# Performance work log

Hardware: AMD Instinct MI355X
Metric: run time of the kernel (lower is better)

The kernel has to match this reference:

```python
import jax, jax.numpy as jnp
import numpy as np

B, N, D, H = 8, 577, 768, 12
HD = D // H
SCALE = HD ** -0.5
LN_EPS = 1e-5


def layer_norm(x, w, b):
    mu = jnp.mean(x, -1, keepdims=True)
    var = jnp.mean((x - mu) ** 2, -1, keepdims=True)
    return (x - mu) * jax.lax.rsqrt(var + LN_EPS) * w + b


def wasserstein_distance_matmul(mean1, cov1, mean2, cov2):
    # all [B,H,N,hd]; returns [B,H,N,N]
    m1_2 = jnp.sum(mean1 ** 2, -1, keepdims=True)
    m2_2 = jnp.sum(mean2 ** 2, -1, keepdims=True)
    ret = -2.0 * jnp.einsum('bhnd,bhmd->bhnm', mean1, mean2) + m1_2 + jnp.swapaxes(m2_2, -1, -2)
    c1s = jnp.sqrt(jnp.clip(cov1, 1e-24))
    c2s = jnp.sqrt(jnp.clip(cov2, 1e-24))
    cov_ret = (-2.0 * jnp.einsum('bhnd,bhmd->bhnm', c1s, c2s)
               + jnp.sum(cov1, -1, keepdims=True)
               + jnp.swapaxes(jnp.sum(cov2, -1, keepdims=True), -1, -2))
    return ret + cov_ret


def setup_inputs() -> dict:
    key = jax.random.key(0)
    ks = jax.random.split(key, 20)
    s = 0.02
    return {
        'x_mean': jax.random.normal(ks[0], (B, N, D), jnp.float32),
        'x_cov': jax.random.normal(ks[1], (B, N, D), jnp.float32),
        'rel_pos_bias': jax.random.normal(ks[2], (1, H, N, N), jnp.float32),
        'norm1_w': jnp.ones((D,), jnp.float32),
        'norm1_b': jnp.zeros((D,), jnp.float32),
        'qkv_w': jax.random.normal(ks[3], (3 * D, D), jnp.float32) * s,
        'proj_w': jax.random.normal(ks[4], (D, D), jnp.float32) * s,
        'proj_b': jnp.zeros((D,), jnp.float32),
        'cov_proj_w': jax.random.normal(ks[5], (D, D), jnp.float32) * s,
        'cov_proj_b': jnp.zeros((D,), jnp.float32),
        'norm2_w': jnp.ones((D,), jnp.float32),
        'norm2_b': jnp.zeros((D,), jnp.float32),
        'fc1_w': jax.random.normal(ks[6], (4 * D, D), jnp.float32) * s,
        'fc1_b': jnp.zeros((4 * D,), jnp.float32),
        'fc2_w': jax.random.normal(ks[7], (D, 4 * D), jnp.float32) * s,
        'fc2_b': jnp.zeros((D,), jnp.float32),
        'gamma1': 0.1 * jnp.ones((D,), jnp.float32),
        'gamma2': 0.1 * jnp.ones((D,), jnp.float32),
    }


def _split_heads(t):
    # [B,N,3D] -> q,k,v each [B,H,N,hd]
    t = t.reshape(B, N, 3, H, HD).transpose(2, 0, 3, 1, 4)
    return t[0], t[1], t[2]


def attention(xm, xc, rel_pos_bias, qkv_w, proj_w, proj_b, cov_proj_w, cov_proj_b):
    qkv = xm @ qkv_w.T                                  # [B,N,3D]
    q, k, v = _split_heads(qkv)
    cov_qkv = jax.nn.elu(xc @ qkv_w.T) + 1.0            # same weights for cov stream
    cov_q, cov_k, cov_v = _split_heads(cov_qkv)
    q = q * SCALE
    attn = -wasserstein_distance_matmul(q, cov_q, k, cov_k)
    attn = jax.nn.sigmoid(attn + 1e-24)
    attn = jax.nn.softmax(attn + rel_pos_bias, axis=-1)  # [B,H,N,N]
    mean_ctx = jnp.einsum('bhnm,bhmd->bhnd', attn, v).transpose(0, 2, 1, 3).reshape(B, N, D)
    cov_ctx = jnp.einsum('bhnm,bhmd->bhnd', attn ** 2, cov_v).transpose(0, 2, 1, 3).reshape(B, N, D)
    mean_out = mean_ctx @ proj_w.T + proj_b
    cov_out = cov_ctx @ cov_proj_w.T + cov_proj_b
    return mean_out, cov_out


def mlp(x, fc1_w, fc1_b, fc2_w, fc2_b):
    h = jax.nn.gelu(x @ fc1_w.T + fc1_b, approximate=False)
    return h @ fc2_w.T + fc2_b


def reference(x_mean, x_cov, rel_pos_bias, norm1_w, norm1_b, qkv_w, proj_w, proj_b,
              cov_proj_w, cov_proj_b, norm2_w, norm2_b, fc1_w, fc1_b, fc2_w, fc2_b,
              gamma1, gamma2):
    mean, cov = attention(layer_norm(x_mean, norm1_w, norm1_b),
                          layer_norm(x_cov, norm1_w, norm1_b),
                          rel_pos_bias, qkv_w, proj_w, proj_b, cov_proj_w, cov_proj_b)
    x_mean = x_mean + gamma1 * mean
    fcm = gamma2 * mlp(layer_norm(x_mean, norm2_w, norm2_b), fc1_w, fc1_b, fc2_w, fc2_b)
    x_cov = x_cov + gamma1 * cov
    fcc = gamma2 * mlp(layer_norm(x_cov, norm2_w, norm2_b), fc1_w, fc1_b, fc2_w, fc2_b)
    return (x_mean + fcm, x_cov + fcc)
```

## Files before the change

### kernel.cpp

```cpp
#include <hip/hip_runtime.h>
#include <hip/hip_bf16.h>
#include <math.h>
#include <stdint.h>

typedef __bf16 bf16;
typedef __attribute__((ext_vector_type(8))) __bf16 bf16x8;
typedef __attribute__((ext_vector_type(4))) float f32x4;

typedef __attribute__((address_space(1))) void gas_void;
typedef __attribute__((address_space(3))) void las_void;

#define DEV __device__ __forceinline__

static constexpr int B_ = 8, N_ = 577, D_ = 768, H_ = 12;
static constexpr int M_ = B_ * N_;
static constexpr int MP_ = 4736;
static constexpr int NP_ = 640;
static constexpr int BH_ = B_ * H_;
static constexpr float SCALE_ = 0.125f;

DEV void async_cp16(const void* g, void* l) {
  __builtin_amdgcn_global_load_lds((gas_void*)g, (las_void*)l, 16, 0, 0);
}
DEV float fast_rcp(float x) { return __builtin_amdgcn_rcpf(x); }
DEV float elu1(float x) { return x > 0.0f ? x + 1.0f : __expf(x); }
DEV float fast_gelu(float x) {
  const float x2 = x * x;
  const float z = x * fmaf(0.0713548826f, x2, 1.5957691216f);
  return x * fast_rcp(1.0f + __expf(-z));
}

__global__ __launch_bounds__(256) void cvt6_kernel(
    const float* __restrict__ s0, const float* __restrict__ s1,
    const float* __restrict__ s2, const float* __restrict__ s3,
    const float* __restrict__ s4, const float* __restrict__ s5,
    bf16* __restrict__ d0, bf16* __restrict__ d1, bf16* __restrict__ d2,
    bf16* __restrict__ d3, bf16* __restrict__ d4, bf16* __restrict__ d5,
    int n0, int n1, int n2, int n3, int n4c, int n5) {
  const float* ss[6] = {s0, s1, s2, s3, s4, s5};
  bf16* dd[6] = {d0, d1, d2, d3, d4, d5};
  const int nn[6] = {n0, n1, n2, n3, n4c, n5};
  int bid = blockIdx.x;
  int seg = 0;
#pragma unroll 6
  for (int k = 0; k < 6; k++) {
    const int nb = (nn[k] + 255) >> 8;
    if (bid < nb) { seg = k; break; }
    bid -= nb;
  }
  const int i = bid * 256 + threadIdx.x;
  if (i < nn[seg]) {
    const float4 v = ((const float4*)ss[seg])[i];
    bf16 o[4] = {(bf16)v.x, (bf16)v.y, (bf16)v.z, (bf16)v.w};
    *(uint64_t*)(dd[seg] + (size_t)i * 4) = *(const uint64_t*)o;
  }
}

__global__ __launch_bounds__(256) void ln2_kernel(
    const float* __restrict__ x0, const float* __restrict__ x1,
    const float* __restrict__ w, const float* __restrict__ bp,
    bf16* __restrict__ out) {
  const int row = blockIdx.x;
  const int st = (int)(row >= M_);
  const int srow = row - st * M_;
  const float* xr = (st ? x1 : x0) + (size_t)srow * D_;
  const int t = threadIdx.x;
  float v0 = xr[t], v1 = xr[t + 256], v2 = xr[t + 512];
  float s = v0 + v1 + v2;
  float ss = v0 * v0 + v1 * v1 + v2 * v2;
#pragma unroll
  for (int m = 32; m >= 1; m >>= 1) {
    s += __shfl_down(s, m);
    ss += __shfl_down(ss, m);
  }
  __shared__ float red[8];
  if ((t & 63) == 0) { red[t >> 6] = s; red[4 + (t >> 6)] = ss; }
  __syncthreads();
  s = red[0] + red[1] + red[2] + red[3];
  ss = red[4] + red[5] + red[6] + red[7];
  const float mu = s * (1.0f / D_);
  float var = ss * (1.0f / D_) - mu * mu;
  var = fmaxf(var, 0.0f);
  const float rs = rsqrtf(var + 1e-5f);
  bf16* orow = out + ((size_t)st * MP_ + srow) * D_;
  orow[t]       = (bf16)((v0 - mu) * rs * w[t]       + bp[t]);
  orow[t + 256] = (bf16)((v1 - mu) * rs * w[t + 256] + bp[t + 256]);
  orow[t + 512] = (bf16)((v2 - mu) * rs * w[t + 512] + bp[t + 512]);
}

enum { EP_BF16 = 0, EP_PROJ = 1, EP_GELU = 2, EP_FC2 = 3 };

template <int EP, int K>
__global__ __launch_bounds__(256) void gemm_bt(
    const bf16* __restrict__ A, const bf16* __restrict__ W0,
    const bf16* __restrict__ W1, int Nn, int gx,
    const float* __restrict__ bias0, const float* __restrict__ bias1,
    const float* __restrict__ gamma,
    const float* __restrict__ resid0, const float* __restrict__ resid1,
    bf16* __restrict__ Cb, float* __restrict__ Cf0, float* __restrict__ Cf1) {
  __shared__ __align__(16) bf16 As[2][128 * 64];
  __shared__ __align__(16) bf16 Bs[2][128 * 64];
  const int nwg = gridDim.x;
  const int o = blockIdx.x;
  const int q = nwg >> 3, r = nwg & 7, xcd = o & 7;
  const int flat = (xcd < r ? xcd * (q + 1) : r * (q + 1) + (xcd - r) * q) + (o >> 3);
  const int gyv = nwg / gx;
  const int fb = gyv >> 2;
  const int bsz = gx << 2;
  int bx, by;
  if (flat < fb * bsz) {
    const int band = flat / bsz, rr2 = flat - band * bsz;
    bx = rr2 >> 2;
    by = band * 4 + (rr2 & 3);
  } else {
    const int rows = gyv - (fb << 2);
    const int rr2 = flat - fb * bsz;
    bx = rr2 / rows;
    by = (fb << 2) + (rr2 - bx * rows);
  }

  const int t = threadIdx.x;
  const int lane = t & 63, wv = t >> 6;
  const int ln = lane & 15, kg = lane >> 4;
  const int wr = wv >> 1, wc = wv & 1;
  const int s = (int)(by >= (MP_ / 128));
  const bf16* W = s ? W1 : W0;
  const size_t brow = (size_t)by * 128;
  const size_t bcol = (size_t)bx * 128;

  const int rA = t >> 3, sl = t & 7;
  const int swsl = (sl ^ (rA & 7)) * 8;
  const bf16* Asrc = A + (brow + rA) * (size_t)K + swsl;
  const bf16* Wsrc = W + (bcol + rA) * (size_t)K + swsl;

  auto stage = [&](int buf, int kk) {
#pragma unroll
    for (int q2 = 0; q2 < 4; q2++) {
      async_cp16(Asrc + (size_t)q2 * 32 * K + kk, &As[buf][(q2 * 256 + wv * 64) * 8]);
      async_cp16(Wsrc + (size_t)q2 * 32 * K + kk, &Bs[buf][(q2 * 256 + wv * 64) * 8]);
    }
  };

  f32x4 acc[4][4] = {};
  constexpr int nt = K >> 6;
  static_assert(K % 64 == 0, "K must be a multiple of 64");
  stage(0, 0);
  __syncthreads();
#pragma unroll 1
  for (int tt = 0; tt < nt; ++tt) {
    if (tt + 1 < nt) stage((tt + 1) & 1, (tt + 1) * 64);
    const int bb = tt & 1;
#pragma unroll
    for (int kh = 0; kh < 2; kh++) {
      bf16x8 af[4], bfr[4];
#pragma unroll
      for (int i = 0; i < 4; i++) {
        const int row = wr * 64 + i * 16 + ln;
        af[i] = *(const bf16x8*)&As[bb][row * 64 + (((kh * 4 + kg) ^ (ln & 7)) * 8)];
      }
#pragma unroll
      for (int j = 0; j < 4; j++) {
        const int row = wc * 64 + j * 16 + ln;
        bfr[j] = *(const bf16x8*)&Bs[bb][row * 64 + (((kh * 4 + kg) ^ (ln & 7)) * 8)];
      }
#pragma unroll
      for (int i = 0; i < 4; i++)
#pragma unroll
        for (int j = 0; j < 4; j++)
          acc[i][j] = __builtin_amdgcn_mfma_f32_16x16x32_bf16(af[i], bfr[j], acc[i][j], 0, 0, 0);
    }
    __syncthreads();
  }

  const float* biasS = s ? bias1 : bias0;
  const float* residS = s ? resid1 : resid0;
  float* CfS = s ? Cf1 : Cf0;
#pragma unroll
  for (int i = 0; i < 4; i++) {
    const int rb = (int)brow + wr * 64 + i * 16 + kg * 4;
#pragma unroll
    for (int j = 0; j < 4; j++) {
      const int col = (int)bcol + wc * 64 + j * 16 + ln;
#pragma unroll
      for (int rr = 0; rr < 4; rr++) {
        const int row = rb + rr;
        float v = acc[i][j][rr];
        if (EP == EP_BF16) {
          Cb[(size_t)row * Nn + col] = (bf16)v;
        } else if (EP == EP_GELU) {
          v += biasS[col];
          Cb[(size_t)row * Nn + col] = (bf16)fast_gelu(v);
        } else {
          const int r2 = row - s * MP_;
          if (r2 < M_) {
            v += biasS[col];
            if (EP == EP_PROJ) {
              CfS[(size_t)r2 * Nn + col] = residS[(size_t)r2 * Nn + col] + gamma[col] * v;
            } else {
              CfS[(size_t)r2 * Nn + col] += gamma[col] * v;
            }
          }
        }
      }
    }
  }
}

__global__ __launch_bounds__(256) void prep_kernel(
    const bf16* __restrict__ qm, const bf16* __restrict__ qc,
    bf16* __restrict__ Qcat, bf16* __restrict__ Kcat,
    bf16* __restrict__ Vt, bf16* __restrict__ CVt,
    float* __restrict__ rowt, float* __restrict__ colt) {
  const int n0 = blockIdx.x * 64;
  const int h = blockIdx.y, b = blockIdx.z;
  const int bh = b * H_ + h;
  const int t = threadIdx.x;
  const int nl = t >> 2, c = t & 3;
  const int n = n0 + nl;
  const bool valid = n < N_;
  __shared__ bf16 vts[64][72], cvts[64][72];
  float q2 = 0.f, cqs = 0.f, k2 = 0.f, cks = 0.f;
  bf16 qo[16], sqo[16], ko[16], sko[16];
  if (valid) {
    const size_t ro = (size_t)(b * N_ + n) * 2304 + h * 64 + c * 16;
#pragma unroll
    for (int half = 0; half < 2; half++) {
      bf16x8 qv8 = *(const bf16x8*)(qm + ro + half * 8);
      bf16x8 kv8 = *(const bf16x8*)(qm + ro + 768 + half * 8);
      bf16x8 vv8 = *(const bf16x8*)(qm + ro + 1536 + half * 8);
      bf16x8 cq8 = *(const bf16x8*)(qc + ro + half * 8);
      bf16x8 ck8 = *(const bf16x8*)(qc + ro + 768 + half * 8);
      bf16x8 cv8 = *(const bf16x8*)(qc + ro + 1536 + half * 8);
#pragma unroll
      for (int i = 0; i < 8; i++) {
        const int d = half * 8 + i;
        float qv = (float)qv8[i] * SCALE_;
        float kv = (float)kv8[i];
        float cq1 = elu1((float)cq8[i]);
        float ck1 = elu1((float)ck8[i]);
        q2 += qv * qv; cqs += cq1; k2 += kv * kv; cks += ck1;
        qo[d] = (bf16)qv; sqo[d] = (bf16)sqrtf(fmaxf(cq1, 1e-24f));
        ko[d] = (bf16)kv; sko[d] = (bf16)sqrtf(fmaxf(ck1, 1e-24f));
        vts[nl][c * 16 + d] = vv8[i];
        cvts[nl][c * 16 + d] = (bf16)elu1((float)cv8[i]);
      }
    }
  } else {
#pragma unroll
    for (int d = 0; d < 16; d++) {
      qo[d] = (bf16)0.f; sqo[d] = (bf16)0.f; ko[d] = (bf16)0.f; sko[d] = (bf16)0.f;
      vts[nl][c * 16 + d] = (bf16)0.f; cvts[nl][c * 16 + d] = (bf16)0.f;
    }
  }
  {
    bf16* qrow = Qcat + ((size_t)bh * NP_ + n) * 128;
    bf16* krow = Kcat + ((size_t)bh * NP_ + n) * 128;
#pragma unroll
    for (int d = 0; d < 16; d++) {
      qrow[c * 16 + d] = qo[d];
      qrow[64 + c * 16 + d] = sqo[d];
      krow[c * 16 + d] = ko[d];
      krow[64 + c * 16 + d] = sko[d];
    }
  }
  float rt = q2 + cqs, ct = k2 + cks;
  rt += __shfl_xor(rt, 1); rt += __shfl_xor(rt, 2);
  ct += __shfl_xor(ct, 1); ct += __shfl_xor(ct, 2);
  if (c == 0) { rowt[(size_t)bh * NP_ + n] = rt; colt[(size_t)bh * NP_ + n] = ct; }
  __syncthreads();
  const int drow = t >> 2;
  const size_t vb = ((size_t)bh * 64 + drow) * NP_ + n0 + c * 16;
#pragma unroll
  for (int i = 0; i < 16; i++) {
    Vt[vb + i] = vts[c * 16 + i][drow];
    CVt[vb + i] = cvts[c * 16 + i][drow];
  }
}

__global__ __launch_bounds__(256) void attn_kernel(
    const bf16* __restrict__ Qcat, const bf16* __restrict__ Kcat,
    const bf16* __restrict__ Vt, const bf16* __restrict__ CVt,
    const float* __restrict__ rowt, const float* __restrict__ colt,
    const bf16* __restrict__ bias,
    bf16* __restrict__ ctxm, bf16* __restrict__ ctxc) {
  const int id = blockIdx.x;
  const int xcd = id & 7, slot = id >> 3;
  const int g = xcd + 8 * (slot / 10);
  const int it = slot % 10;
  const int b = g / H_, h = g % H_;
  const int bh = g;
  const int i0 = it * 64;
  const int t = threadIdx.x;
  const int lane = t & 63, w = t >> 6;
  const int ln = lane & 15, kg = lane >> 4;
  __shared__ __align__(16) bf16 Ks[2][64 * 128];
  __shared__ __align__(16) bf16 Vs[2][64 * 64];
  __shared__ __align__(16) bf16 CVs[2][64 * 64];
  __shared__ __align__(16) bf16 Ps[64 * 72];

  const bf16* Qg = Qcat + (size_t)bh * NP_ * 128;
  const bf16* Kg = Kcat + (size_t)bh * NP_ * 128;
  const bf16* Vg = Vt + (size_t)bh * 64 * NP_;
  const bf16* CVg = CVt + (size_t)bh * 64 * NP_;

  auto stageK = [&](int buf, int j0) {
#pragma unroll
    for (int qq = 0; qq < 4; qq++) {
      const int idx = qq * 256 + t;
      const int row = idx >> 4, sl = idx & 15;
      async_cp16(Kg + (size_t)(j0 + row) * 128 + ((sl ^ (row & 7)) * 8),
                 &Ks[buf][(qq * 256 + w * 64) * 8]);
    }
  };
  auto stageV = [&](int buf, int j0) {
#pragma unroll
    for (int qq = 0; qq < 2; qq++) {
      const int idx = qq * 256 + t;
      const int row = idx >> 3, sl = idx & 7;
      async_cp16(Vg + (size_t)row * NP_ + j0 + ((sl ^ (row & 7)) * 8),
                 &Vs[buf][(qq * 256 + w * 64) * 8]);
      async_cp16(CVg + (size_t)row * NP_ + j0 + ((sl ^ (row & 7)) * 8),
                 &CVs[buf][(qq * 256 + w * 64) * 8]);
    }
  };

#pragma unroll
  for (int qq = 0; qq < 4; qq++) {
    const int idx = qq * 256 + t;
    const int row = idx >> 4, sl = idx & 15;
    async_cp16(Qg + (size_t)(i0 + row) * 128 + ((sl ^ (row & 7)) * 8),
               &Ks[0][(qq * 256 + w * 64) * 8]);
  }
  stageK(1, 0);
  stageV(0, 0);
  __syncthreads();
  bf16x8 aq[4];
  {
    const int row = w * 16 + ln;
#pragma unroll
    for (int kc = 0; kc < 4; kc++) {
      const int slot2 = kc * 4 + kg;
      aq[kc] = *(const bf16x8*)&Ks[0][row * 128 + ((slot2 ^ (row & 7)) * 8)];
    }
  }
  float rt[4];
#pragma unroll
  for (int r = 0; r < 4; r++) rt[r] = rowt[(size_t)bh * NP_ + i0 + w * 16 + kg * 4 + r];
  __syncthreads();

  f32x4 accm[4] = {}, accc[4] = {};
  float den[4] = {0.f, 0.f, 0.f, 0.f};
  const int igb = i0 + w * 16 + kg * 4;

  for (int jt = 0; jt < 10; jt++) {
    const int j0 = jt * 64;
    const int kc2 = (jt + 1) & 1;
    const int vc2 = jt & 1;
    if (jt + 1 < 10) {
      stageK(jt & 1, j0 + 64);
      stageV((jt + 1) & 1, j0 + 64);
    }
    float bb[4][4], ctb[4];
#pragma unroll
    for (int js = 0; js < 4; js++) {
      const int jg = j0 + js * 16 + ln;
      const int jc = jg < N_ ? jg : N_ - 1;
      ctb[js] = colt[(size_t)bh * NP_ + jg];
#pragma unroll
      for (int r = 0; r < 4; r++) {
        const int ic = (igb + r) < N_ ? (igb + r) : N_ - 1;
        bb[js][r] = (float)bias[((size_t)h * N_ + ic) * N_ + jc];
      }
    }
#pragma unroll
    for (int js = 0; js < 4; js++) {
      f32x4 sv = {};
#pragma unroll
      for (int kc = 0; kc < 4; kc++) {
        const int row = js * 16 + ln;
        const int slot2 = kc * 4 + kg;
        bf16x8 bk = *(const bf16x8*)&Ks[kc2][row * 128 + ((slot2 ^ (row & 7)) * 8)];
        sv = __builtin_amdgcn_mfma_f32_16x16x32_bf16(aq[kc], bk, sv, 0, 0, 0);
      }
      const int jg = j0 + js * 16 + ln;
#pragma unroll
      for (int r = 0; r < 4; r++) {
        const float S = 2.0f * sv[r] - rt[r] - ctb[js];
        const float sig = fast_rcp(1.0f + __expf(-S));
        float e = __expf(sig + bb[js][r]);
        if (jg >= N_) e = 0.0f;
        const bf16 eb = (bf16)e;
        den[r] += (float)eb;
        Ps[(w * 16 + kg * 4 + r) * 72 + js * 16 + ln] = eb;
      }
    }
#pragma unroll
    for (int ks = 0; ks < 2; ks++) {
      const int prow = w * 16 + ln;
      bf16x8 pa = *(const bf16x8*)&Ps[prow * 72 + ks * 32 + kg * 8];
      bf16x8 p2a;
#pragma unroll
      for (int i = 0; i < 8; i++) {
        const float pf = (float)pa[i];
        p2a[i] = (bf16)(pf * pf);
      }
#pragma unroll
      for (int nt = 0; nt < 4; nt++) {
        const int vrow = nt * 16 + ln;
        const int slot2 = ks * 4 + kg;
        bf16x8 vb = *(const bf16x8*)&Vs[vc2][vrow * 64 + ((slot2 ^ (vrow & 7)) * 8)];
        bf16x8 cvb = *(const bf16x8*)&CVs[vc2][vrow * 64 + ((slot2 ^ (vrow & 7)) * 8)];
        accm[nt] = __builtin_amdgcn_mfma_f32_16x16x32_bf16(pa, vb, accm[nt], 0, 0, 0);
        accc[nt] = __builtin_amdgcn_mfma_f32_16x16x32_bf16(p2a, cvb, accc[nt], 0, 0, 0);
      }
    }
    __syncthreads();
  }
#pragma unroll
  for (int r = 0; r < 4; r++) {
    float d = den[r];
    d += __shfl_xor(d, 1); d += __shfl_xor(d, 2);
    d += __shfl_xor(d, 4); d += __shfl_xor(d, 8);
    den[r] = d;
  }
#pragma unroll
  for (int r = 0; r < 4; r++) {
    const int ig = i0 + w * 16 + kg * 4 + r;
    if (ig < N_) {
      const float inv = fast_rcp(den[r]);
      const float inv2 = inv * inv;
      const size_t base = (size_t)(b * N_ + ig) * D_ + h * 64;
#pragma unroll
      for (int nt = 0; nt < 4; nt++) {
        ctxm[base + nt * 16 + ln] = (bf16)(accm[nt][r] * inv);
        ctxc[base + nt * 16 + ln] = (bf16)(accc[nt][r] * inv2);
      }
    }
  }
}

extern "C" void kernel_launch(void* const* d_in, const int* in_sizes, int n_in,
                              void* d_out, int out_size, void* d_ws, size_t ws_size,
                              hipStream_t stream) {
  const float* x_mean = (const float*)d_in[0];
  const float* x_cov  = (const float*)d_in[1];
  const float* rpb    = (const float*)d_in[2];
  const float* n1w    = (const float*)d_in[3];
  const float* n1b    = (const float*)d_in[4];
  const float* qkvw   = (const float*)d_in[5];
  const float* projw  = (const float*)d_in[6];
  const float* projb  = (const float*)d_in[7];
  const float* cprojw = (const float*)d_in[8];
  const float* cprojb = (const float*)d_in[9];
  const float* n2w    = (const float*)d_in[10];
  const float* n2b    = (const float*)d_in[11];
  const float* fc1w   = (const float*)d_in[12];
  const float* fc1b   = (const float*)d_in[13];
  const float* fc2w   = (const float*)d_in[14];
  const float* fc2b   = (const float*)d_in[15];
  const float* g1     = (const float*)d_in[16];
  const float* g2     = (const float*)d_in[17];
  (void)in_sizes; (void)n_in; (void)out_size; (void)ws_size;

  char* ws = (char*)d_ws;
  size_t off = 0;
  auto take = [&](size_t bytes) {
    char* p = ws + off;
    off += (bytes + 255) & ~(size_t)255;
    return p;
  };
  bf16* wq   = (bf16*)take((size_t)2304 * 768 * 2);
  bf16* wp   = (bf16*)take((size_t)768 * 768 * 2);
  bf16* wcp  = (bf16*)take((size_t)768 * 768 * 2);
  bf16* wf1  = (bf16*)take((size_t)3072 * 768 * 2);
  bf16* wf2  = (bf16*)take((size_t)768 * 3072 * 2);
  bf16* xln  = (bf16*)take((size_t)2 * MP_ * 768 * 2);
  char* R    = take((size_t)2 * MP_ * 3072 * 2);
  bf16* qkvb = (bf16*)R;
  bf16* hbuf = (bf16*)R;
  bf16* biasb = (bf16*)(R + (size_t)2 * MP_ * 2304 * 2);
  bf16* Qcat = (bf16*)take((size_t)BH_ * NP_ * 128 * 2);
  bf16* Kcat = (bf16*)take((size_t)BH_ * NP_ * 128 * 2);
  bf16* Vt   = (bf16*)take((size_t)BH_ * 64 * NP_ * 2);
  bf16* CVt  = (bf16*)take((size_t)BH_ * 64 * NP_ * 2);
  float* rowt = (float*)take((size_t)BH_ * NP_ * 4);
  float* colt = (float*)take((size_t)BH_ * NP_ * 4);
  bf16* ctx  = (bf16*)take((size_t)2 * MP_ * 768 * 2);

  float* outm = (float*)d_out;
  float* outc = outm + (size_t)M_ * D_;

  {
    const int c0 = 2304 * 768 / 4, c1 = 768 * 768 / 4, c2 = 768 * 768 / 4;
    const int c3 = 3072 * 768 / 4, c4 = 768 * 3072 / 4, c5 = H_ * N_ * N_ / 4;
    const int nb = ((c0 + 255) >> 8) + ((c1 + 255) >> 8) + ((c2 + 255) >> 8) +
                   ((c3 + 255) >> 8) + ((c4 + 255) >> 8) + ((c5 + 255) >> 8);
    cvt6_kernel<<<nb, 256, 0, stream>>>(qkvw, projw, cprojw, fc1w, fc2w, rpb,
                                        wq, wp, wcp, wf1, wf2, biasb,
                                        c0, c1, c2, c3, c4, c5);
  }
  ln2_kernel<<<2 * M_, 256, 0, stream>>>(x_mean, x_cov, n1w, n1b, xln);
  gemm_bt<EP_BF16, 768><<<18 * 74, 256, 0, stream>>>(xln, wq, wq, 2304, 18,
      nullptr, nullptr, nullptr, nullptr, nullptr, qkvb, nullptr, nullptr);
  prep_kernel<<<dim3(10, 12, 8), 256, 0, stream>>>(
      qkvb, qkvb + (size_t)MP_ * 2304, Qcat, Kcat, Vt, CVt, rowt, colt);
  attn_kernel<<<960, 256, 0, stream>>>(Qcat, Kcat, Vt, CVt, rowt, colt, biasb,
                                       ctx, ctx + (size_t)MP_ * 768);
  gemm_bt<EP_PROJ, 768><<<6 * 74, 256, 0, stream>>>(ctx, wp, wcp, 768, 6,
      projb, cprojb, g1, x_mean, x_cov, nullptr, outm, outc);
  ln2_kernel<<<2 * M_, 256, 0, stream>>>(outm, outc, n2w, n2b, xln);
  gemm_bt<EP_GELU, 768><<<24 * 74, 256, 0, stream>>>(xln, wf1, wf1, 3072, 24,
      fc1b, fc1b, nullptr, nullptr, nullptr, hbuf, nullptr, nullptr);
  gemm_bt<EP_FC2, 3072><<<6 * 74, 256, 0, stream>>>(hbuf, wf2, wf2, 768, 6,
      fc2b, fc2b, g2, nullptr, nullptr, nullptr, outm, outc);
}
```

Before: 349.0 us.

## Process 128 query rows per attention block to reuse staged K/V tiles

```diff
diff --git a/kernel.cpp b/kernel.cpp
--- a/kernel.cpp
+++ b/kernel.cpp
@@ -285,11 +285,11 @@
     bf16* __restrict__ ctxm, bf16* __restrict__ ctxc) {
   const int id = blockIdx.x;
   const int xcd = id & 7, slot = id >> 3;
-  const int g = xcd + 8 * (slot / 10);
-  const int it = slot % 10;
+  const int g = xcd + 8 * (slot / 5);
+  const int it = slot % 5;
   const int b = g / H_, h = g % H_;
   const int bh = g;
-  const int i0 = it * 64;
+  const int i0 = it * 128;
   const int t = threadIdx.x;
   const int lane = t & 63, w = t >> 6;
   const int ln = lane & 15, kg = lane >> 4;
@@ -325,32 +325,39 @@
   };
 
 #pragma unroll
-  for (int qq = 0; qq < 4; qq++) {
-    const int idx = qq * 256 + t;
-    const int row = idx >> 4, sl = idx & 15;
-    async_cp16(Qg + (size_t)(i0 + row) * 128 + ((sl ^ (row & 7)) * 8),
-               &Ks[0][(qq * 256 + w * 64) * 8]);
-  }
+  for (int hf = 0; hf < 2; hf++) {
+#pragma unroll
+    for (int qq = 0; qq < 4; qq++) {
+      const int idx = qq * 256 + t;
+      const int row = idx >> 4, sl = idx & 15;
+      async_cp16(Qg + (size_t)(i0 + hf * 64 + row) * 128 + ((sl ^ (row & 7)) * 8),
+                 &Ks[hf][(qq * 256 + w * 64) * 8]);
+    }
+  }
+  __syncthreads();
+  bf16x8 aq[2][4];
+#pragma unroll
+  for (int hf = 0; hf < 2; hf++) {
+    const int row = w * 16 + ln;
+#pragma unroll
+    for (int kc = 0; kc < 4; kc++) {
+      const int slot2 = kc * 4 + kg;
+      aq[hf][kc] = *(const bf16x8*)&Ks[hf][row * 128 + ((slot2 ^ (row & 7)) * 8)];
+    }
+  }
+  float rt2[2][4];
+#pragma unroll
+  for (int hf = 0; hf < 2; hf++)
+#pragma unroll
+    for (int r = 0; r < 4; r++)
+      rt2[hf][r] = rowt[(size_t)bh * NP_ + i0 + hf * 64 + w * 16 + kg * 4 + r];
+  __syncthreads();
   stageK(1, 0);
   stageV(0, 0);
   __syncthreads();
-  bf16x8 aq[4];
-  {
-    const int row = w * 16 + ln;
-#pragma unroll
-    for (int kc = 0; kc < 4; kc++) {
-      const int slot2 = kc * 4 + kg;
-      aq[kc] = *(const bf16x8*)&Ks[0][row * 128 + ((slot2 ^ (row & 7)) * 8)];
-    }
-  }
-  float rt[4];
-#pragma unroll
-  for (int r = 0; r < 4; r++) rt[r] = rowt[(size_t)bh * NP_ + i0 + w * 16 + kg * 4 + r];
-  __syncthreads();
-
-  f32x4 accm[4] = {}, accc[4] = {};
-  float den[4] = {0.f, 0.f, 0.f, 0.f};
-  const int igb = i0 + w * 16 + kg * 4;
+
+  f32x4 accm[2][4] = {}, accc[2][4] = {};
+  float den[2][4] = {};
 
   for (int jt = 0; jt < 10; jt++) {
     const int j0 = jt * 64;
@@ -360,83 +367,94 @@
       stageK(jt & 1, j0 + 64);
       stageV((jt + 1) & 1, j0 + 64);
     }
-    float bb[4][4], ctb[4];
-#pragma unroll
-    for (int js = 0; js < 4; js++) {
-      const int jg = j0 + js * 16 + ln;
-      const int jc = jg < N_ ? jg : N_ - 1;
-      ctb[js] = colt[(size_t)bh * NP_ + jg];
-#pragma unroll
-      for (int r = 0; r < 4; r++) {
-        const int ic = (igb + r) < N_ ? (igb + r) : N_ - 1;
-        bb[js][r] = (float)bias[((size_t)h * N_ + ic) * N_ + jc];
-      }
-    }
-#pragma unroll
-    for (int js = 0; js < 4; js++) {
-      f32x4 sv = {};
-#pragma unroll
-      for (int kc = 0; kc < 4; kc++) {
-        const int row = js * 16 + ln;
-        const int slot2 = kc * 4 + kg;
-        bf16x8 bk = *(const bf16x8*)&Ks[kc2][row * 128 + ((slot2 ^ (row & 7)) * 8)];
-        sv = __builtin_amdgcn_mfma_f32_16x16x32_bf16(aq[kc], bk, sv, 0, 0, 0);
-      }
-      const int jg = j0 + js * 16 + ln;
-#pragma unroll
-      for (int r = 0; r < 4; r++) {
-        const float S = 2.0f * sv[r] - rt[r] - ctb[js];
-        const float sig = fast_rcp(1.0f + __expf(-S));
-        float e = __expf(sig + bb[js][r]);
-        if (jg >= N_) e = 0.0f;
-        const bf16 eb = (bf16)e;
-        den[r] += (float)eb;
-        Ps[(w * 16 + kg * 4 + r) * 72 + js * 16 + ln] = eb;
-      }
-    }
-#pragma unroll
-    for (int ks = 0; ks < 2; ks++) {
-      const int prow = w * 16 + ln;
-      bf16x8 pa = *(const bf16x8*)&Ps[prow * 72 + ks * 32 + kg * 8];
-      bf16x8 p2a;
-#pragma unroll
-      for (int i = 0; i < 8; i++) {
-        const float pf = (float)pa[i];
-        p2a[i] = (bf16)(pf * pf);
-      }
-#pragma unroll
-      for (int nt = 0; nt < 4; nt++) {
-        const int vrow = nt * 16 + ln;
-        const int slot2 = ks * 4 + kg;
-        bf16x8 vb = *(const bf16x8*)&Vs[vc2][vrow * 64 + ((slot2 ^ (vrow & 7)) * 8)];
-        bf16x8 cvb = *(const bf16x8*)&CVs[vc2][vrow * 64 + ((slot2 ^ (vrow & 7)) * 8)];
-        accm[nt] = __builtin_amdgcn_mfma_f32_16x16x32_bf16(pa, vb, accm[nt], 0, 0, 0);
-        accc[nt] = __builtin_amdgcn_mfma_f32_16x16x32_bf16(p2a, cvb, accc[nt], 0, 0, 0);
+    float ctb[4];
+#pragma unroll
+    for (int js = 0; js < 4; js++)
+      ctb[js] = colt[(size_t)bh * NP_ + j0 + js * 16 + ln];
+#pragma unroll
+    for (int hf = 0; hf < 2; hf++) {
+      const int igb = i0 + hf * 64 + w * 16 + kg * 4;
+      float bb[4][4];
+#pragma unroll
+      for (int js = 0; js < 4; js++) {
+        const int jg = j0 + js * 16 + ln;
+        const int jc = jg < N_ ? jg : N_ - 1;
+#pragma unroll
+        for (int r = 0; r < 4; r++) {
+          const int ic = (igb + r) < N_ ? (igb + r) : N_ - 1;
+          bb[js][r] = (float)bias[((size_t)h * N_ + ic) * N_ + jc];
+        }
+      }
+#pragma unroll
+      for (int js = 0; js < 4; js++) {
+        f32x4 sv = {};
+#pragma unroll
+        for (int kc = 0; kc < 4; kc++) {
+          const int row = js * 16 + ln;
+          const int slot2 = kc * 4 + kg;
+          bf16x8 bk = *(const bf16x8*)&Ks[kc2][row * 128 + ((slot2 ^ (row & 7)) * 8)];
+          sv = __builtin_amdgcn_mfma_f32_16x16x32_bf16(aq[hf][kc], bk, sv, 0, 0, 0);
+        }
+        const int jg = j0 + js * 16 + ln;
+#pragma unroll
+        for (int r = 0; r < 4; r++) {
+          const float S = 2.0f * sv[r] - rt2[hf][r] - ctb[js];
+          const float sig = fast_rcp(1.0f + __expf(-S));
+          float e = __expf(sig + bb[js][r]);
+          if (jg >= N_) e = 0.0f;
+          const bf16 eb = (bf16)e;
+          den[hf][r] += (float)eb;
+          Ps[(w * 16 + kg * 4 + r) * 72 + js * 16 + ln] = eb;
+        }
+      }
+#pragma unroll
+      for (int ks = 0; ks < 2; ks++) {
+        const int prow = w * 16 + ln;
+        bf16x8 pa = *(const bf16x8*)&Ps[prow * 72 + ks * 32 + kg * 8];
+        bf16x8 p2a;
+#pragma unroll
+        for (int i = 0; i < 8; i++) {
+          const float pf = (float)pa[i];
+          p2a[i] = (bf16)(pf * pf);
+        }
+#pragma unroll
+        for (int nt = 0; nt < 4; nt++) {
+          const int vrow = nt * 16 + ln;
+          const int slot2 = ks * 4 + kg;
+          bf16x8 vb = *(const bf16x8*)&Vs[vc2][vrow * 64 + ((slot2 ^ (vrow & 7)) * 8)];
+          bf16x8 cvb = *(const bf16x8*)&CVs[vc2][vrow * 64 + ((slot2 ^ (vrow & 7)) * 8)];
+          accm[hf][nt] = __builtin_amdgcn_mfma_f32_16x16x32_bf16(pa, vb, accm[hf][nt], 0, 0, 0);
+          accc[hf][nt] = __builtin_amdgcn_mfma_f32_16x16x32_bf16(p2a, cvb, accc[hf][nt], 0, 0, 0);
+        }
       }
     }
     __syncthreads();
   }
 #pragma unroll
-  for (int r = 0; r < 4; r++) {
-    float d = den[r];
-    d += __shfl_xor(d, 1); d += __shfl_xor(d, 2);
-    d += __shfl_xor(d, 4); d += __shfl_xor(d, 8);
-    den[r] = d;
-  }
-#pragma unroll
-  for (int r = 0; r < 4; r++) {
-    const int ig = i0 + w * 16 + kg * 4 + r;
-    if (ig < N_) {
-      const float inv = fast_rcp(den[r]);
-      const float inv2 = inv * inv;
-      const size_t base = (size_t)(b * N_ + ig) * D_ + h * 64;
-#pragma unroll
-      for (int nt = 0; nt < 4; nt++) {
-        ctxm[base + nt * 16 + ln] = (bf16)(accm[nt][r] * inv);
-        ctxc[base + nt * 16 + ln] = (bf16)(accc[nt][r] * inv2);
-      }
-    }
-  }
+  for (int hf = 0; hf < 2; hf++)
+#pragma unroll
+    for (int r = 0; r < 4; r++) {
+      float d = den[hf][r];
+      d += __shfl_xor(d, 1); d += __shfl_xor(d, 2);
+      d += __shfl_xor(d, 4); d += __shfl_xor(d, 8);
+      den[hf][r] = d;
+    }
+#pragma unroll
+  for (int hf = 0; hf < 2; hf++)
+#pragma unroll
+    for (int r = 0; r < 4; r++) {
+      const int ig = i0 + hf * 64 + w * 16 + kg * 4 + r;
+      if (ig < N_) {
+        const float inv = fast_rcp(den[hf][r]);
+        const float inv2 = inv * inv;
+        const size_t base = (size_t)(b * N_ + ig) * D_ + h * 64;
+#pragma unroll
+        for (int nt = 0; nt < 4; nt++) {
+          ctxm[base + nt * 16 + ln] = (bf16)(accm[hf][nt][r] * inv);
+          ctxc[base + nt * 16 + ln] = (bf16)(accc[hf][nt][r] * inv2);
+        }
+      }
+    }
 }
 
 extern "C" void kernel_launch(void* const* d_in, const int* in_sizes, int n_in,
@@ -504,7 +522,7 @@
       nullptr, nullptr, nullptr, nullptr, nullptr, qkvb, nullptr, nullptr);
   prep_kernel<<<dim3(10, 12, 8), 256, 0, stream>>>(
       qkvb, qkvb + (size_t)MP_ * 2304, Qcat, Kcat, Vt, CVt, rowt, colt);
-  attn_kernel<<<960, 256, 0, stream>>>(Qcat, Kcat, Vt, CVt, rowt, colt, biasb,
+  attn_kernel<<<480, 256, 0, stream>>>(Qcat, Kcat, Vt, CVt, rowt, colt, biasb,
                                        ctx, ctx + (size_t)MP_ * 768);
   gemm_bt<EP_PROJ, 768><<<6 * 74, 256, 0, stream>>>(ctx, wp, wcp, 768, 6,
       projb, cprojb, g1, x_mean, x_cov, nullptr, outm, outc);
```

Measured after the change: 405.4 us. 1.16x slower.
